# Performance work log

Hardware: AMD Instinct MI355X
Metric: run time of the kernel (lower is better)

Reference implementation:

```python
import jax, jax.numpy as jnp
import numpy as np

KS = 3
PAD = 1


def setup_inputs() -> dict:
    key = jax.random.key(0)
    k1, k2, k3 = jax.random.split(key, 3)
    x = jax.random.normal(k1, (8, 64, 96, 96), dtype=jnp.float32)
    offset = jax.random.normal(k2, (8, 18, 96, 96), dtype=jnp.float32)
    W = jax.random.normal(k3, (64, 64, 3, 3), dtype=jnp.float32) * 0.05
    return {"x": x, "offset": offset, "W": W}


def _deform_conv(x, offset, W):
    ks, pad = KS, PAD
    b, c, H, Wd = x.shape
    N = offset.shape[1] // 2  # ks*ks
    h, w = offset.shape[2], offset.shape[3]
    xp = jnp.pad(x, ((0, 0), (0, 0), (pad, pad), (pad, pad)))
    hp, wp = H + 2 * pad, Wd + 2 * pad

    # p = p_0 + p_n + offset, permuted to [b, h, w, 2N]
    r = jnp.arange(-(ks - 1) // 2, (ks - 1) // 2 + 1)
    pn_x, pn_y = jnp.meshgrid(r, r, indexing="ij")
    p_n = jnp.concatenate([pn_x.ravel(), pn_y.ravel()]).reshape(1, 2 * N, 1, 1).astype(offset.dtype)
    p0x, p0y = jnp.meshgrid(jnp.arange(1, h + 1), jnp.arange(1, w + 1), indexing="ij")
    p_0 = jnp.concatenate(
        [jnp.broadcast_to(p0x[None, None], (1, N, h, w)),
         jnp.broadcast_to(p0y[None, None], (1, N, h, w))], axis=1
    ).astype(offset.dtype)
    p = jnp.transpose(p_0 + p_n + offset, (0, 2, 3, 1))  # [b,h,w,2N]
    px, py = p[..., :N], p[..., N:]

    fx, fy = jnp.floor(px), jnp.floor(py)
    q_lt_x = jnp.clip(fx, 0, hp - 1)
    q_lt_y = jnp.clip(fy, 0, wp - 1)
    q_rb_x = jnp.clip(fx + 1, 0, hp - 1)
    q_rb_y = jnp.clip(fy + 1, 0, wp - 1)

    # out-of-image mask (computed on unclamped p, as in original)
    mx = ((px < pad) | (px > hp - 1 - pad)).astype(px.dtype)
    my = ((py < pad) | (py > wp - 1 - pad)).astype(py.dtype)
    px = jnp.clip(px * (1 - mx) + fx * mx, 0, hp - 1)
    py = jnp.clip(py * (1 - my) + fy * my, 0, wp - 1)

    g_lt = (1 + (q_lt_x - px)) * (1 + (q_lt_y - py))
    g_rb = (1 - (q_rb_x - px)) * (1 - (q_rb_y - py))
    g_lb = (1 + (q_lt_x - px)) * (1 - (q_rb_y - py))
    g_rt = (1 - (q_rb_x - px)) * (1 + (q_lt_y - py))

    x_flat = xp.reshape(b, c, hp * wp)

    def gather(qx, qy):
        idx = (qx.astype(jnp.int32) * wp + qy.astype(jnp.int32)).reshape(b, -1)
        g = jax.vmap(lambda xf, ix: xf[:, ix])(x_flat, idx)
        return g.reshape(b, c, h, w, N)

    x_off = (g_lt[:, None] * gather(q_lt_x, q_lt_y)
             + g_rb[:, None] * gather(q_rb_x, q_rb_y)
             + g_lb[:, None] * gather(q_lt_x, q_rb_y)
             + g_rt[:, None] * gather(q_rb_x, q_lt_y))  # [b,c,h,w,N]

    # reshape: out[:,:, i*ks+ki, j*ks+kj] = x_off[:,:,i,j, ki*ks+kj]
    x_off = x_off.reshape(b, c, h, w, ks, ks)
    x_off = jnp.transpose(x_off, (0, 1, 2, 4, 3, 5)).reshape(b, c, h * ks, w * ks)

    return jax.lax.conv_general_dilated(
        x_off, W, window_strides=(ks, ks), padding="VALID",
        dimension_numbers=("NCHW", "OIHW", "NCHW"))


def reference(x, offset, W):
    return _deform_conv(x, offset, W)
```

## Files before the change

kernel.cpp:

```cpp
#include <hip/hip_runtime.h>


typedef __bf16 bf16_t;
typedef __bf16 bf16x8 __attribute__((ext_vector_type(8)));
typedef float  f32x4  __attribute__((ext_vector_type(4)));

#define NB 8
#define NC 64
#define NO 64
#define NH 96
#define NW 96
#define HP 98
#define NPT 9
#define PIX 64
#define ASTR 72

struct DCParams { int u0, u1, v0, v1; float glt, grb, glb, grt; };

__device__ __forceinline__ DCParams dc_params(const float* __restrict__ off, int b, int i, int j, int n) {
    const int a = n / 3, b2 = n % 3;
    const float offx = off[((size_t)(b * 18 + n) * NH + i) * NW + j];
    const float offy = off[((size_t)(b * 18 + 9 + n) * NH + i) * NW + j];
    float px = (float)(i + a) + offx;
    float py = (float)(j + b2) + offy;
    const float fx = floorf(px), fy = floorf(py);
    const float x0 = fminf(fmaxf(fx, 0.f), 97.f);
    const float x1 = fminf(fmaxf(fx + 1.f, 0.f), 97.f);
    const float y0 = fminf(fmaxf(fy, 0.f), 97.f);
    const float y1 = fminf(fmaxf(fy + 1.f, 0.f), 97.f);
    px = (px < 1.f || px > 96.f) ? x0 : px;
    py = (py < 1.f || py > 96.f) ? y0 : py;
    const float wx0 = 1.f + x0 - px;
    const float wx1 = 1.f - x1 + px;
    const float wy0 = 1.f + y0 - py;
    const float wy1 = 1.f - y1 + py;
    DCParams p;
    p.u0 = (int)x0; p.u1 = (int)x1; p.v0 = (int)y0; p.v1 = (int)y1;
    p.glt = wx0 * wy0; p.grb = wx1 * wy1; p.glb = wx0 * wy1; p.grt = wx1 * wy0;
    return p;
}

__global__ __launch_bounds__(256) void zero_xt_pinned(uint4* __restrict__ xt4) {
    const int b = blockIdx.x & 7;
    const int idx = (blockIdx.x >> 3) * 256 + threadIdx.x;
    if (idx < (HP * HP * NC * 2 / 16)) {
        uint4 z = {0, 0, 0, 0};
        xt4[(size_t)b * (HP * HP * NC * 2 / 16) + idx] = z;
    }
}

__global__ __launch_bounds__(256) void fill_xt16(const float* __restrict__ x, bf16_t* __restrict__ xt) {
    __shared__ float tile[64][17];
    const int blk = blockIdx.x;
    const int b  = blk & 7;
    const int r  = blk >> 3;
    const int jt = r % 6;
    const int i  = r / 6;
    const int j0 = jt * 16;
    const int t = threadIdx.x;
    {
        const int jj = t & 15, cq = t >> 4;
        #pragma unroll
        for (int rr = 0; rr < 4; ++rr) {
            const int c = cq * 4 + rr;
            tile[c][jj] = x[(((size_t)b * NC + c) * NH + i) * NW + j0 + jj];
        }
    }
    __syncthreads();
    {
        const int c = t & 63, jq = t >> 6;
        #pragma unroll
        for (int rr = 0; rr < 4; ++rr) {
            const int jj = jq * 4 + rr;
            xt[(((size_t)b * HP + (i + 1)) * HP + (j0 + jj + 1)) * NC + c] = (bf16_t)tile[c][jj];
        }
    }
}

__global__ __launch_bounds__(256) void make_bt(const float* __restrict__ W, bf16_t* __restrict__ Bt) {
    int t = blockIdx.x * 256 + threadIdx.x;
    if (t < NPT * NC * NO) {
        const int j = t & 7, l = (t >> 3) & 63, frag = t >> 9;
        const int nt = frag & 3, kk = (frag >> 2) & 1, n = frag >> 3;
        const int o = nt * 16 + (l & 15);
        const int c = kk * 32 + 8 * (l >> 4) + j;
        Bt[t] = (bf16_t)W[(size_t)o * 576 + c * 9 + n];
    }
}

__device__ __forceinline__ void mfma_tap(const bf16_t* sAbuf, const bf16_t* __restrict__ Bt,
                                         int n, int w, int l, f32x4 acc[4]) {
    const int mrow = l & 15, khi = l >> 4;
    #pragma unroll
    for (int kk = 0; kk < 2; ++kk) {
        const bf16x8 bf = *(const bf16x8*)(Bt + (size_t)(((n * 2 + kk) * 4 + w)) * 512 + l * 8);
        #pragma unroll
        for (int mt = 0; mt < 4; ++mt) {
            const bf16x8 af = *(const bf16x8*)(sAbuf + (mt * 16 + mrow) * ASTR + kk * 32 + khi * 8);
            acc[mt] = __builtin_amdgcn_mfma_f32_16x16x32_bf16(af, bf, acc[mt], 0, 0, 0);
        }
    }
}

__global__ __launch_bounds__(256) void deform_mfma(const bf16_t* __restrict__ xt, const bf16_t* __restrict__ Bt,
                                                   const float* __restrict__ off, float* __restrict__ out) {
    __shared__ __align__(16) unsigned char smem[NO * 68 * 4];
    bf16_t* sA = (bf16_t*)smem;
    float*  sO = (float*)smem;
    __shared__ __align__(16) int4   sI[2][PIX];
    __shared__ __align__(16) float4 sG[2][PIX];

    const int t = threadIdx.x;
    const int l = t & 63;
    const int w = t >> 6;
    const int bid = blockIdx.x;
    const int b  = bid & 7;
    const int pb = (bid >> 3) * PIX;

    const int pl   = l >> 3;
    const int slot = l & 7;
    const bf16_t* ibase = xt + (size_t)b * (HP * HP * NC) + slot * 8;

    f32x4 acc[4] = {};
    bf16x8 d[2][4];

    if (t < PIX) {
        const int pp = pb + t, ii = pp / 96, jj = pp - (pp / 96) * 96;
        const DCParams p = dc_params(off, b, ii, jj, 0);
        sI[0][t] = make_int4((p.u0 * HP + p.v0) * NC, (p.u1 * HP + p.v1) * NC,
                             (p.u0 * HP + p.v1) * NC, (p.u1 * HP + p.v0) * NC);
        sG[0][t] = make_float4(p.glt, p.grb, p.glb, p.grt);
    }
    __syncthreads();
    #pragma unroll
    for (int q = 0; q < 2; ++q) {
        const int px = w * 16 + pl + 8 * q;
        const int4 a4 = sI[0][px];
        d[q][0] = *(const bf16x8*)(ibase + a4.x);
        d[q][1] = *(const bf16x8*)(ibase + a4.y);
        d[q][2] = *(const bf16x8*)(ibase + a4.z);
        d[q][3] = *(const bf16x8*)(ibase + a4.w);
    }

    for (int n = 0; n < NPT; ++n) {
        __syncthreads();
        #pragma unroll
        for (int q = 0; q < 2; ++q) {
            const int px = w * 16 + pl + 8 * q;
            const float4 g = sG[n & 1][px];
            bf16x8 r;
            #pragma unroll
            for (int e = 0; e < 8; ++e) {
                const float v = g.x * (float)d[q][0][e] + g.y * (float)d[q][1][e]
                              + g.z * (float)d[q][2][e] + g.w * (float)d[q][3][e];
                r[e] = (bf16_t)v;
            }
            *(bf16x8*)(sA + px * ASTR + slot * 8) = r;
        }
        if (n + 1 < NPT && t < PIX) {
            const int pp = pb + t, ii = pp / 96, jj = pp - (pp / 96) * 96;
            const DCParams p = dc_params(off, b, ii, jj, n + 1);
            sI[(n + 1) & 1][t] = make_int4((p.u0 * HP + p.v0) * NC, (p.u1 * HP + p.v1) * NC,
                                           (p.u0 * HP + p.v1) * NC, (p.u1 * HP + p.v0) * NC);
            sG[(n + 1) & 1][t] = make_float4(p.glt, p.grb, p.glb, p.grt);
        }
        __syncthreads();
        if (n + 1 < NPT) {
            #pragma unroll
            for (int q = 0; q < 2; ++q) {
                const int px = w * 16 + pl + 8 * q;
                const int4 a4 = sI[(n + 1) & 1][px];
                d[q][0] = *(const bf16x8*)(ibase + a4.x);
                d[q][1] = *(const bf16x8*)(ibase + a4.y);
                d[q][2] = *(const bf16x8*)(ibase + a4.z);
                d[q][3] = *(const bf16x8*)(ibase + a4.w);
            }
        }
        mfma_tap(sA, Bt, n, w, l, acc);
    }

    __syncthreads();

    const int orow = w * 16 + (l & 15);
    #pragma unroll
    for (int mt = 0; mt < 4; ++mt)
        #pragma unroll
        for (int r = 0; r < 4; ++r)
            sO[orow * 68 + mt * 16 + (l >> 4) * 4 + r] = acc[mt][r];
    __syncthreads();

    const int o = t >> 2, q = t & 3;
    float4* dst = (float4*)(out + ((size_t)(b * NO + o)) * (NH * NW) + pb + q * 16);
    const float* src = sO + o * 68 + q * 16;
    #pragma unroll
    for (int k2 = 0; k2 < 4; ++k2) dst[k2] = ((const float4*)src)[k2];
}

__global__ __launch_bounds__(256) void deform_naive(const float* __restrict__ x, const float* __restrict__ W,
                                                    const float* __restrict__ off, float* __restrict__ out) {
    __shared__ float sv[576];
    __shared__ DCParams sp[NPT];
    const int t = threadIdx.x;
    const int P = blockIdx.x;
    const int b = P / (NH * NW), pp = P - b * (NH * NW);
    const int i = pp / 96, j = pp - (pp / 96) * 96;
    if (t < NPT) sp[t] = dc_params(off, b, i, j, t);
    __syncthreads();
    for (int k = t; k < 576; k += 256) {
        const int c = k / 9, n = k - c * 9;
        const DCParams p = sp[n];
        const float* xb = x + ((size_t)(b * NC + c)) * (NH * NW);
        const float vlt = (p.u0 >= 1 && p.u0 <= 96 && p.v0 >= 1 && p.v0 <= 96) ? xb[(p.u0 - 1) * 96 + (p.v0 - 1)] : 0.f;
        const float vrb = (p.u1 >= 1 && p.u1 <= 96 && p.v1 >= 1 && p.v1 <= 96) ? xb[(p.u1 - 1) * 96 + (p.v1 - 1)] : 0.f;
        const float vlb = (p.u0 >= 1 && p.u0 <= 96 && p.v1 >= 1 && p.v1 <= 96) ? xb[(p.u0 - 1) * 96 + (p.v1 - 1)] : 0.f;
        const float vrt = (p.u1 >= 1 && p.u1 <= 96 && p.v0 >= 1 && p.v0 <= 96) ? xb[(p.u1 - 1) * 96 + (p.v0 - 1)] : 0.f;
        sv[k] = p.glt * vlt + p.grb * vrb + p.glb * vlb + p.grt * vrt;
    }
    __syncthreads();
    if (t < NO) {
        const float* wrow = W + (size_t)t * 576;
        float acc = 0.f;
        for (int k = 0; k < 576; ++k) acc += sv[k] * wrow[k];
        out[((size_t)(b * NO + t)) * (NH * NW) + pp] = acc;
    }
}

extern "C" void kernel_launch(void* const* d_in, const int* in_sizes, int n_in,
                              void* d_out, int out_size, void* d_ws, size_t ws_size,
                              hipStream_t stream) {
    const float* x   = (const float*)d_in[0];
    const float* off = (const float*)d_in[1];
    const float* W   = (const float*)d_in[2];
    float* out = (float*)d_out;

    const size_t XT_ELEMS = (size_t)NB * HP * HP * NC;
    const size_t XT_BYTES = XT_ELEMS * 2;
    const size_t BT_ELEMS = (size_t)NPT * NC * NO;
    const size_t need = XT_BYTES + BT_ELEMS * 2;

    if (ws_size >= need) {
        bf16_t* xt = (bf16_t*)d_ws;
        bf16_t* Bt = (bf16_t*)((char*)d_ws + XT_BYTES);
        const int per_img_u4 = (int)(HP * HP * NC * 2 / 16);
        const int zblocks = ((per_img_u4 + 255) / 256) * 8;
        zero_xt_pinned<<<dim3(zblocks), dim3(256), 0, stream>>>((uint4*)xt);
        make_bt<<<dim3(144), dim3(256), 0, stream>>>(W, Bt);
        fill_xt16<<<dim3(NB * 96 * 6), dim3(256), 0, stream>>>(x, xt);
        deform_mfma<<<dim3(NB * NH * NW / PIX), dim3(256), 0, stream>>>(xt, Bt, off, out);
    } else {
        deform_naive<<<dim3(NB * NH * NW), dim3(256), 0, stream>>>(x, W, off, out);
    }
}
```

Before: 44.13 us.

## Fuse prep kernels, zero only padding border, double-buffer sA in deform loop

Merges the three preprocessing launches (zeroing, weight packing, NHWC bf16 transpose) into one kernel. Instead of zeroing the whole padded image, it now zeroes only the one-pixel border, and the weight pack writes 8 bf16 values per thread as a single vector. The main kernel double-buffers the shared A tile, which removes one barrier per tap. This cuts launch overhead and redundant memory writes, at the cost of more shared memory and a write-after-read hazard on the alternating buffers that relies on the remaining barrier.

```diff
diff --git a/kernel.cpp b/kernel.cpp
--- a/kernel.cpp
+++ b/kernel.cpp
@@ -40,51 +40,62 @@
     return p;
 }
 
-__global__ __launch_bounds__(256) void zero_xt_pinned(uint4* __restrict__ xt4) {
-    const int b = blockIdx.x & 7;
-    const int idx = (blockIdx.x >> 3) * 256 + threadIdx.x;
-    if (idx < (HP * HP * NC * 2 / 16)) {
-        uint4 z = {0, 0, 0, 0};
-        xt4[(size_t)b * (HP * HP * NC * 2 / 16) + idx] = z;
-    }
-}
-
-__global__ __launch_bounds__(256) void fill_xt16(const float* __restrict__ x, bf16_t* __restrict__ xt) {
+__global__ __launch_bounds__(256) void prep_all(const float* __restrict__ x, const float* __restrict__ W,
+                                                bf16_t* __restrict__ xt, bf16_t* __restrict__ Bt) {
     __shared__ float tile[64][17];
     const int blk = blockIdx.x;
-    const int b  = blk & 7;
-    const int r  = blk >> 3;
-    const int jt = r % 6;
-    const int i  = r / 6;
-    const int j0 = jt * 16;
+    const int b = blk & 7;
+    const int r = blk >> 3;
     const int t = threadIdx.x;
-    {
-        const int jj = t & 15, cq = t >> 4;
-        #pragma unroll
-        for (int rr = 0; rr < 4; ++rr) {
-            const int c = cq * 4 + rr;
-            tile[c][jj] = x[(((size_t)b * NC + c) * NH + i) * NW + j0 + jj];
-        }
-    }
-    __syncthreads();
-    {
-        const int c = t & 63, jq = t >> 6;
-        #pragma unroll
-        for (int rr = 0; rr < 4; ++rr) {
-            const int jj = jq * 4 + rr;
-            xt[(((size_t)b * HP + (i + 1)) * HP + (j0 + jj + 1)) * NC + c] = (bf16_t)tile[c][jj];
-        }
-    }
-}
-
-__global__ __launch_bounds__(256) void make_bt(const float* __restrict__ W, bf16_t* __restrict__ Bt) {
-    int t = blockIdx.x * 256 + threadIdx.x;
-    if (t < NPT * NC * NO) {
-        const int j = t & 7, l = (t >> 3) & 63, frag = t >> 9;
+
+    if (r < 576) {
+        const int jt = r % 6;
+        const int i  = r / 6;
+        const int j0 = jt * 16;
+        {
+            const int jj = t & 15, cq = t >> 4;
+            #pragma unroll
+            for (int rr = 0; rr < 4; ++rr) {
+                const int c = cq * 4 + rr;
+                tile[c][jj] = x[(((size_t)b * NC + c) * NH + i) * NW + j0 + jj];
+            }
+        }
+        __syncthreads();
+        {
+            const int c = t & 63, jq = t >> 6;
+            #pragma unroll
+            for (int rr = 0; rr < 4; ++rr) {
+                const int jj = jq * 4 + rr;
+                xt[(((size_t)b * HP + (i + 1)) * HP + (j0 + jj + 1)) * NC + c] = (bf16_t)tile[c][jj];
+            }
+        }
+    } else if (r < 592) {
+        const int idx = (r - 576) * 256 + t;
+        uint4* xt4 = (uint4*)xt;
+        const size_t ib = (size_t)b * (HP * HP * NC / 8);
+        const uint4 z = {0, 0, 0, 0};
+        if (idx < 1568) {
+            const int u   = (idx < 784) ? 0 : 97;
+            const int pos = (idx < 784) ? idx : idx - 784;
+            xt4[ib + (size_t)u * 784 + pos] = z;
+        } else if (idx < 3104) {
+            const int k  = idx - 1568;
+            const int v  = (k < 768) ? 0 : 97;
+            const int kk = (k < 768) ? k : k - 768;
+            const int u  = 1 + (kk >> 3), c8 = kk & 7;
+            xt4[ib + (size_t)(u * HP + v) * 8 + c8] = z;
+        }
+    } else if (b == 0) {
+        const int idx = (r - 592) * 256 + t;
+        const int l = idx & 63, frag = idx >> 6;
         const int nt = frag & 3, kk = (frag >> 2) & 1, n = frag >> 3;
-        const int o = nt * 16 + (l & 15);
-        const int c = kk * 32 + 8 * (l >> 4) + j;
-        Bt[t] = (bf16_t)W[(size_t)o * 576 + c * 9 + n];
+        const int o  = nt * 16 + (l & 15);
+        const int cb = kk * 32 + 8 * (l >> 4);
+        bf16x8 v;
+        #pragma unroll
+        for (int j = 0; j < 8; ++j)
+            v[j] = (bf16_t)W[(size_t)o * 576 + (cb + j) * 9 + n];
+        *(bf16x8*)(Bt + (size_t)idx * 8) = v;
     }
 }
 
@@ -104,7 +115,7 @@
 
 __global__ __launch_bounds__(256) void deform_mfma(const bf16_t* __restrict__ xt, const bf16_t* __restrict__ Bt,
                                                    const float* __restrict__ off, float* __restrict__ out) {
-    __shared__ __align__(16) unsigned char smem[NO * 68 * 4];
+    __shared__ __align__(16) unsigned char smem[2 * PIX * ASTR * 2];
     bf16_t* sA = (bf16_t*)smem;
     float*  sO = (float*)smem;
     __shared__ __align__(16) int4   sI[2][PIX];
@@ -143,19 +154,19 @@
     }
 
     for (int n = 0; n < NPT; ++n) {
-        __syncthreads();
+        bf16_t* buf = sA + (n & 1) * (PIX * ASTR);
         #pragma unroll
         for (int q = 0; q < 2; ++q) {
             const int px = w * 16 + pl + 8 * q;
             const float4 g = sG[n & 1][px];
-            bf16x8 r;
+            bf16x8 rv;
             #pragma unroll
             for (int e = 0; e < 8; ++e) {
                 const float v = g.x * (float)d[q][0][e] + g.y * (float)d[q][1][e]
                               + g.z * (float)d[q][2][e] + g.w * (float)d[q][3][e];
-                r[e] = (bf16_t)v;
-            }
-            *(bf16x8*)(sA + px * ASTR + slot * 8) = r;
+                rv[e] = (bf16_t)v;
+            }
+            *(bf16x8*)(buf + px * ASTR + slot * 8) = rv;
         }
         if (n + 1 < NPT && t < PIX) {
             const int pp = pb + t, ii = pp / 96, jj = pp - (pp / 96) * 96;
@@ -176,7 +187,7 @@
                 d[q][3] = *(const bf16x8*)(ibase + a4.w);
             }
         }
-        mfma_tap(sA, Bt, n, w, l, acc);
+        mfma_tap(buf, Bt, n, w, l, acc);
     }
 
     __syncthreads();
@@ -241,11 +252,7 @@
     if (ws_size >= need) {
         bf16_t* xt = (bf16_t*)d_ws;
         bf16_t* Bt = (bf16_t*)((char*)d_ws + XT_BYTES);
-        const int per_img_u4 = (int)(HP * HP * NC * 2 / 16);
-        const int zblocks = ((per_img_u4 + 255) / 256) * 8;
-        zero_xt_pinned<<<dim3(zblocks), dim3(256), 0, stream>>>((uint4*)xt);
-        make_bt<<<dim3(144), dim3(256), 0, stream>>>(W, Bt);
-        fill_xt16<<<dim3(NB * 96 * 6), dim3(256), 0, stream>>>(x, xt);
+        prep_all<<<dim3(8 * 610), dim3(256), 0, stream>>>(x, W, xt, Bt);
         deform_mfma<<<dim3(NB * NH * NW / PIX), dim3(256), 0, stream>>>(xt, Bt, off, out);
     } else {
         deform_naive<<<dim3(NB * NH * NW), dim3(256), 0, stream>>>(x, W, off, out);
```

New measurement: 38.24 us, median of 3. 1.15x faster.
